# Kernel tuning notes

Measured on AMD Instinct MI355X. Metric: run time of the kernel, lower is better.

Reference implementation:

```python
import jax, jax.numpy as jnp
import numpy as np

B, T, F = 2048, 60, 89
H = 1024
OUT = 30  # output_predicted_chords


def setup_inputs() -> dict:
    key = jax.random.key(0)
    k1, k2, k3, k4 = jax.random.split(key, 4)
    # small init scale keeps the relu-activated recurrence numerically stable
    s = 0.02
    return {
        "x": jax.random.normal(k1, (B, T, F), dtype=jnp.float32),
        "W": jax.random.normal(k2, (F, 4 * H), dtype=jnp.float32) * s,
        "U": jax.random.normal(k3, (H, 4 * H), dtype=jnp.float32) * s,
        "b": jnp.zeros((4 * H,), dtype=jnp.float32),
        "Wd": jax.random.normal(k4, (H, OUT), dtype=jnp.float32) * s,
        "bd": jnp.zeros((OUT,), dtype=jnp.float32),
    }


def _lstm_last_h(x, W, U, b):
    """Keras LSTM(activation='relu', recurrent_activation='sigmoid').
    Gate order in Keras kernels: i, f, c (candidate), o.
    Returns last hidden state h_T of shape [B, H]."""
    Bsz = x.shape[0]
    Hdim = U.shape[0]
    # precompute input projections for all timesteps: [T, B, 4H]
    xz = jnp.einsum('btf,fg->tbg', x, W) + b

    def step(carry, xz_t):
        h, c = carry
        z = xz_t + h @ U                      # [B, 4H]
        i, f, g, o = jnp.split(z, 4, axis=-1)
        i = jax.nn.sigmoid(i)
        f = jax.nn.sigmoid(f)
        g = jax.nn.relu(g)                    # activation='relu' on candidate
        o = jax.nn.sigmoid(o)
        c = f * c + i * g
        h = o * jax.nn.relu(c)                # activation='relu' on cell output
        return (h, c), None

    h0 = jnp.zeros((Bsz, Hdim), dtype=x.dtype)
    c0 = jnp.zeros((Bsz, Hdim), dtype=x.dtype)
    (hT, _), _ = jax.lax.scan(step, (h0, c0), xz)
    return hT


def reference(x, W, U, b, Wd, bd):
    # LSTM(return_sequences=True) then take x[:, -1, :] == last hidden state
    hT = _lstm_last_h(x, W, U, b)             # [B, H]
    y = hT @ Wd + bd                           # [B, OUT]
    return y.reshape(-1, OUT, 1)               # [B, 30, 1]
```

## Files before the change

### kernel.cpp

```cpp
#include <hip/hip_runtime.h>
#include <cstdint>
#include <cstddef>

#define Bsz 2048
#define Tseq 60
#define Fin 89
#define Hd 1024
#define G4 4096
#define KX 96
#define NOUT 30

typedef _Float16 half8 __attribute__((ext_vector_type(8)));
typedef float f32x4 __attribute__((ext_vector_type(4)));

template <int N> struct IC { static constexpr int value = N; };

__device__ __forceinline__ void gload_lds16(const void* g, void* l) {
  __builtin_amdgcn_global_load_lds((const __attribute__((address_space(1))) void*)g,
                                   (__attribute__((address_space(3))) void*)l,
                                   16, 0, 0);
}

__device__ __forceinline__ float sigmoidf_fast(float x) {
  return 1.0f / (1.0f + __expf(-x));
}


__global__ __launch_bounds__(256) void convert_x(const float* __restrict__ x,
                                                 _Float16* __restrict__ xp) {
  int idx = blockIdx.x * 256 + threadIdx.x;
  int k = idx % KX;
  int b = (idx / KX) % Bsz;
  int t = idx / (KX * Bsz);
  float v = (k < Fin) ? x[((size_t)b * Tseq + t) * Fin + k] : 0.0f;
  xp[idx] = (_Float16)v;
}

__global__ __launch_bounds__(256) void transpose_W(const float* __restrict__ W,
                                                   _Float16* __restrict__ Wpt) {
  __shared__ float tile[32][33];
  int n0 = blockIdx.x * 32;
  int k0 = blockIdx.y * 32;
  int tx = threadIdx.x, ty = threadIdx.y;
  for (int i = ty; i < 32; i += 8) {
    int k = k0 + i;
    tile[i][tx] = (k < Fin) ? W[(size_t)k * G4 + n0 + tx] : 0.0f;
  }
  __syncthreads();
  for (int i = ty; i < 32; i += 8)
    Wpt[(size_t)(n0 + i) * KX + k0 + tx] = (_Float16)tile[tx][i];
}

__global__ __launch_bounds__(256) void transpose_U(const float* __restrict__ U,
                                                   _Float16* __restrict__ Upt) {
  __shared__ float tile[32][33];
  int n0 = blockIdx.x * 32;
  int k0 = blockIdx.y * 32;
  int tx = threadIdx.x, ty = threadIdx.y;
  for (int i = ty; i < 32; i += 8)
    tile[i][tx] = U[(size_t)(k0 + i) * G4 + n0 + tx];
  __syncthreads();
  for (int i = ty; i < 32; i += 8)
    Upt[(size_t)(n0 + i) * Hd + k0 + tx] = (_Float16)tile[tx][i];
}

__global__ __launch_bounds__(256, 2) void lstm_step(
    const _Float16* __restrict__ xp_t,
    const _Float16* __restrict__ Wpt,
    const _Float16* __restrict__ Upt,
    const float*    __restrict__ bias,
    const _Float16* __restrict__ h_in,
    _Float16*       __restrict__ h_out,
    float*          __restrict__ cst,
    int skip_h)
{
  __shared__ __align__(16) _Float16 As[3 * 4096];
  __shared__ __align__(16) _Float16 Bs[3 * 4096];

  const int tid  = threadIdx.x;
  const int wave = tid >> 6;
  const int lane = tid & 63;
  const int quad = lane >> 4;
  const int l16  = lane & 15;
  const int m0 = blockIdx.x * 128;
  const int j0 = blockIdx.y * 32;

  const int srow = lane >> 2;
  const int qg   = (lane & 3) ^ ((lane >> 3) & 3);
  const int sA   = quad ^ ((l16 >> 1) & 3);

  const int hb    = 16 * (wave & 1);
  const int mwave = 64 * (wave >> 1);
  const int j  = j0 + hb + l16;
  const int uA = 4 * (wave >> 1);
  const int uB = wave & 1;
  const int aoff = l16 * 32 + sA * 8;

  float bv[4];
  for (int p = 0; p < 4; ++p) bv[p] = bias[p * Hd + j];

  f32x4 acc[4][4];
  for (int mi = 0; mi < 4; ++mi)
    for (int p = 0; p < 4; ++p)
      acc[mi][p] = f32x4{bv[p], bv[p], bv[p], bv[p]};

  auto round = [&](auto ncI, const _Float16* __restrict__ Ab, int strA,
                   const _Float16* __restrict__ Bb, int strB, int k0) {
    constexpr int NC = decltype(ncI)::value;
    __syncthreads();
#pragma unroll
    for (int ii = 0; ii < NC * 2; ++ii) {
      int i = ii * 4 + wave;
      int st = i >> 3, ci = i & 7;
      gload_lds16(Ab + (size_t)(m0 + ci * 16 + srow) * strA + k0 + st * 32 + qg * 8,
                  &As[st * 4096 + ci * 512]);
    }
#pragma unroll
    for (int ii = 0; ii < NC * 2; ++ii) {
      int i = ii * 4 + wave;
      int st = i >> 3, ci = i & 7;
      int ln = ci * 16 + srow;
      int gn = (ln >> 5) * Hd + j0 + (ln & 31);
      gload_lds16(Bb + (size_t)gn * strB + k0 + st * 32 + qg * 8,
                  &Bs[st * 4096 + ci * 512]);
    }
    __syncthreads();
#pragma unroll
    for (int st = 0; st < NC; ++st) {
      half8 a[4], bq[4];
      for (int mi = 0; mi < 4; ++mi)
        a[mi] = *(const half8*)&As[st * 4096 + (uA + mi) * 512 + aoff];
      for (int p = 0; p < 4; ++p)
        bq[p] = *(const half8*)&Bs[st * 4096 + (2 * p + uB) * 512 + aoff];
      for (int mi = 0; mi < 4; ++mi)
        for (int p = 0; p < 4; ++p)
          acc[mi][p] = __builtin_amdgcn_mfma_f32_16x16x32_f16(a[mi], bq[p],
                                                              acc[mi][p],
                                                              0, 0, 0);
    }
  };

  round(IC<3>{}, xp_t, KX, Wpt, KX, 0);

  if (!skip_h) {
    for (int r = 0; r < 16; ++r)
      round(IC<2>{}, h_in, Hd, Upt, Hd, r * 64);
  }

  for (int mi = 0; mi < 4; ++mi) {
    for (int r = 0; r < 4; ++r) {
      int row = m0 + mwave + mi * 16 + quad * 4 + r;
      size_t idx = (size_t)row * Hd + j;
      float iv = sigmoidf_fast(acc[mi][0][r]);
      float fv = sigmoidf_fast(acc[mi][1][r]);
      float gv = fmaxf(acc[mi][2][r], 0.0f);
      float ov = sigmoidf_fast(acc[mi][3][r]);
      float cprev = skip_h ? 0.0f : cst[idx];
      float cv = fv * cprev + iv * gv;
      cst[idx] = cv;
      float hv = ov * fmaxf(cv, 0.0f);
      h_out[idx] = (_Float16)hv;
    }
  }
}

__global__ __launch_bounds__(256) void final_dense(const _Float16* __restrict__ h,
                                                   const float* __restrict__ Wd,
                                                   const float* __restrict__ bd,
                                                   float* __restrict__ y) {
  __shared__ float hs[Hd];
  __shared__ float red[8][32];
  int bi = blockIdx.x;
  for (int k = threadIdx.x; k < Hd; k += 256)
    hs[k] = (float)h[(size_t)bi * Hd + k];
  __syncthreads();
  int o  = threadIdx.x & 31;
  int ch = threadIdx.x >> 5;
  float p = 0.0f;
  if (o < NOUT) {
    int k0 = ch * (Hd / 8);
    for (int k = k0; k < k0 + (Hd / 8); ++k)
      p += hs[k] * Wd[(size_t)k * NOUT + o];
  }
  red[ch][o] = p;
  __syncthreads();
  if (threadIdx.x < NOUT) {
    float s = bd[threadIdx.x];
    for (int c2 = 0; c2 < 8; ++c2) s += red[c2][threadIdx.x];
    y[(size_t)bi * NOUT + threadIdx.x] = s;
  }
}


extern "C" void kernel_launch(void* const* d_in, const int* in_sizes, int n_in,
                              void* d_out, int out_size, void* d_ws, size_t ws_size,
                              hipStream_t stream) {
  const float* x  = (const float*)d_in[0];
  const float* W  = (const float*)d_in[1];
  const float* U  = (const float*)d_in[2];
  const float* b  = (const float*)d_in[3];
  const float* Wd = (const float*)d_in[4];
  const float* bd = (const float*)d_in[5];
  float* y = (float*)d_out;

  char* ws = (char*)d_ws;
  _Float16* xp  = (_Float16*)ws; ws += (size_t)Tseq * Bsz * KX * 2;
  _Float16* Wpt = (_Float16*)ws; ws += (size_t)G4 * KX * 2;
  _Float16* Upt = (_Float16*)ws; ws += (size_t)G4 * Hd * 2;
  _Float16* hb0 = (_Float16*)ws; ws += (size_t)Bsz * Hd * 2;
  _Float16* hb1 = (_Float16*)ws; ws += (size_t)Bsz * Hd * 2;
  float*    cst = (float*)ws;    ws += (size_t)Bsz * Hd * 4;

  convert_x<<<(Tseq * Bsz * KX) / 256, 256, 0, stream>>>(x, xp);
  transpose_W<<<dim3(G4 / 32, KX / 32), dim3(32, 8), 0, stream>>>(W, Wpt);
  transpose_U<<<dim3(G4 / 32, Hd / 32), dim3(32, 8), 0, stream>>>(U, Upt);

  for (int t = 0; t < Tseq; ++t) {
    const _Float16* hin  = ((t - 1) & 1) ? hb1 : hb0;
    _Float16*       hout = (t & 1) ? hb1 : hb0;
    lstm_step<<<dim3(Bsz / 128, G4 / 128), 256, 0, stream>>>(
        xp + (size_t)t * (Bsz * KX), Wpt, Upt, b,
        (t == 0) ? hb0 : hin, hout, cst, (t == 0) ? 1 : 0);
  }

  final_dense<<<Bsz, 256, 0, stream>>>(hb1, Wd, bd, y);
}
```

Before: 1.714 ms.

## Double-buffer LDS K-loop in LSTM step and remap blocks for XCD locality

The per-step GEMM now uses two LDS buffers, issuing the async global-to-LDS loads for the next K chunk while MFMAs run on the current one. This removes the two barriers per round that previously serialized load and compute. The input dimension is padded from 96 to 128 so the x-projection fits the same 64-wide chunk shape, which adds some wasted MFMA work and memory traffic. The grid is flattened and block ids are swizzled so consecutive blocks on the same XCD share B-row tiles, aiming at better L2 reuse. LDS per block grows from 48KB to 64KB, which may affect occupancy at 2 blocks per CU.

Result: no change. 1.736 ms (+1.3%).

```diff
diff --git a/kernel.cpp b/kernel.cpp
--- a/kernel.cpp
+++ b/kernel.cpp
@@ -7,13 +7,11 @@
 #define Fin 89
 #define Hd 1024
 #define G4 4096
-#define KX 96
+#define KXP 128
 #define NOUT 30
 
 typedef _Float16 half8 __attribute__((ext_vector_type(8)));
 typedef float f32x4 __attribute__((ext_vector_type(4)));
-
-template <int N> struct IC { static constexpr int value = N; };
 
 __device__ __forceinline__ void gload_lds16(const void* g, void* l) {
   __builtin_amdgcn_global_load_lds((const __attribute__((address_space(1))) void*)g,
@@ -29,9 +27,9 @@
 __global__ __launch_bounds__(256) void convert_x(const float* __restrict__ x,
                                                  _Float16* __restrict__ xp) {
   int idx = blockIdx.x * 256 + threadIdx.x;
-  int k = idx % KX;
-  int b = (idx / KX) % Bsz;
-  int t = idx / (KX * Bsz);
+  int k = idx % KXP;
+  int b = (idx / KXP) % Bsz;
+  int t = idx / (KXP * Bsz);
   float v = (k < Fin) ? x[((size_t)b * Tseq + t) * Fin + k] : 0.0f;
   xp[idx] = (_Float16)v;
 }
@@ -48,7 +46,7 @@
   }
   __syncthreads();
   for (int i = ty; i < 32; i += 8)
-    Wpt[(size_t)(n0 + i) * KX + k0 + tx] = (_Float16)tile[tx][i];
+    Wpt[(size_t)(n0 + i) * KXP + k0 + tx] = (_Float16)tile[tx][i];
 }
 
 __global__ __launch_bounds__(256) void transpose_U(const float* __restrict__ U,
@@ -74,16 +72,19 @@
     float*          __restrict__ cst,
     int skip_h)
 {
-  __shared__ __align__(16) _Float16 As[3 * 4096];
-  __shared__ __align__(16) _Float16 Bs[3 * 4096];
+  __shared__ __align__(16) _Float16 As[2 * 8192];
+  __shared__ __align__(16) _Float16 Bs[2 * 8192];
 
   const int tid  = threadIdx.x;
   const int wave = tid >> 6;
   const int lane = tid & 63;
   const int quad = lane >> 4;
   const int l16  = lane & 15;
-  const int m0 = blockIdx.x * 128;
-  const int j0 = blockIdx.y * 32;
+
+  const int id   = blockIdx.x;
+  const int virt = (id & 7) * 64 + (id >> 3);
+  const int m0 = (virt & 15) * 128;
+  const int j0 = (virt >> 4) * 32;
 
   const int srow = lane >> 2;
   const int qg   = (lane & 3) ^ ((lane >> 3) & 3);
@@ -104,34 +105,38 @@
     for (int p = 0; p < 4; ++p)
       acc[mi][p] = f32x4{bv[p], bv[p], bv[p], bv[p]};
 
-  auto round = [&](auto ncI, const _Float16* __restrict__ Ab, int strA,
-                   const _Float16* __restrict__ Bb, int strB, int k0) {
-    constexpr int NC = decltype(ncI)::value;
-    __syncthreads();
+  auto stage = [&](int buf, int r) {
+    const _Float16* Ab; const _Float16* Bb; int strA, strB, k0;
+    if (r < 2) { Ab = xp_t; strA = KXP; Bb = Wpt; strB = KXP; k0 = r * 64; }
+    else       { Ab = h_in; strA = Hd;  Bb = Upt; strB = Hd;  k0 = (r - 2) * 64; }
+    _Float16* Ad = &As[buf * 8192];
+    _Float16* Bd = &Bs[buf * 8192];
 #pragma unroll
-    for (int ii = 0; ii < NC * 2; ++ii) {
+    for (int ii = 0; ii < 4; ++ii) {
       int i = ii * 4 + wave;
       int st = i >> 3, ci = i & 7;
       gload_lds16(Ab + (size_t)(m0 + ci * 16 + srow) * strA + k0 + st * 32 + qg * 8,
-                  &As[st * 4096 + ci * 512]);
+                  Ad + st * 4096 + ci * 512);
     }
 #pragma unroll
-    for (int ii = 0; ii < NC * 2; ++ii) {
+    for (int ii = 0; ii < 4; ++ii) {
       int i = ii * 4 + wave;
       int st = i >> 3, ci = i & 7;
       int ln = ci * 16 + srow;
       int gn = (ln >> 5) * Hd + j0 + (ln & 31);
       gload_lds16(Bb + (size_t)gn * strB + k0 + st * 32 + qg * 8,
-                  &Bs[st * 4096 + ci * 512]);
-    }
-    __syncthreads();
+                  Bd + st * 4096 + ci * 512);
+    }
+  };
+
+  auto compute = [&](int buf) {
 #pragma unroll
-    for (int st = 0; st < NC; ++st) {
+    for (int st = 0; st < 2; ++st) {
       half8 a[4], bq[4];
       for (int mi = 0; mi < 4; ++mi)
-        a[mi] = *(const half8*)&As[st * 4096 + (uA + mi) * 512 + aoff];
+        a[mi] = *(const half8*)&As[buf * 8192 + st * 4096 + (uA + mi) * 512 + aoff];
       for (int p = 0; p < 4; ++p)
-        bq[p] = *(const half8*)&Bs[st * 4096 + (2 * p + uB) * 512 + aoff];
+        bq[p] = *(const half8*)&Bs[buf * 8192 + st * 4096 + (2 * p + uB) * 512 + aoff];
       for (int mi = 0; mi < 4; ++mi)
         for (int p = 0; p < 4; ++p)
           acc[mi][p] = __builtin_amdgcn_mfma_f32_16x16x32_f16(a[mi], bq[p],
@@ -140,11 +145,16 @@
     }
   };
 
-  round(IC<3>{}, xp_t, KX, Wpt, KX, 0);
-
-  if (!skip_h) {
-    for (int r = 0; r < 16; ++r)
-      round(IC<2>{}, h_in, Hd, Upt, Hd, r * 64);
+  const int NR = skip_h ? 2 : 18;
+  stage(0, 0);
+  __syncthreads();
+  for (int r = 0; r < NR; r += 2) {
+    if (r + 1 < NR) stage(1, r + 1);
+    compute(0);
+    __syncthreads();
+    if (r + 2 < NR) stage(0, r + 2);
+    compute(1);
+    __syncthreads();
   }
 
   for (int mi = 0; mi < 4; ++mi) {
@@ -204,22 +214,22 @@
   float* y = (float*)d_out;
 
   char* ws = (char*)d_ws;
-  _Float16* xp  = (_Float16*)ws; ws += (size_t)Tseq * Bsz * KX * 2;
-  _Float16* Wpt = (_Float16*)ws; ws += (size_t)G4 * KX * 2;
+  _Float16* xp  = (_Float16*)ws; ws += (size_t)Tseq * Bsz * KXP * 2;
+  _Float16* Wpt = (_Float16*)ws; ws += (size_t)G4 * KXP * 2;
   _Float16* Upt = (_Float16*)ws; ws += (size_t)G4 * Hd * 2;
   _Float16* hb0 = (_Float16*)ws; ws += (size_t)Bsz * Hd * 2;
   _Float16* hb1 = (_Float16*)ws; ws += (size_t)Bsz * Hd * 2;
   float*    cst = (float*)ws;    ws += (size_t)Bsz * Hd * 4;
 
-  convert_x<<<(Tseq * Bsz * KX) / 256, 256, 0, stream>>>(x, xp);
-  transpose_W<<<dim3(G4 / 32, KX / 32), dim3(32, 8), 0, stream>>>(W, Wpt);
+  convert_x<<<(Tseq * Bsz * KXP) / 256, 256, 0, stream>>>(x, xp);
+  transpose_W<<<dim3(G4 / 32, KXP / 32), dim3(32, 8), 0, stream>>>(W, Wpt);
   transpose_U<<<dim3(G4 / 32, Hd / 32), dim3(32, 8), 0, stream>>>(U, Upt);
 
   for (int t = 0; t < Tseq; ++t) {
     const _Float16* hin  = ((t - 1) & 1) ? hb1 : hb0;
     _Float16*       hout = (t & 1) ? hb1 : hb0;
-    lstm_step<<<dim3(Bsz / 128, G4 / 128), 256, 0, stream>>>(
-        xp + (size_t)t * (Bsz * KX), Wpt, Upt, b,
+    lstm_step<<<dim3((Bsz / 128) * (G4 / 128)), 256, 0, stream>>>(
+        xp + (size_t)t * (Bsz * KXP), Wpt, Upt, b,
         (t == 0) ? hb0 : hin, hout, cst, (t == 0) ? 1 : 0);
   }
 
```
